# Performance work log

Measured on AMD Instinct MI355X. Metric: run time of the kernel, lower is better.

## Reference

```python
import jax, jax.numpy as jnp
import numpy as np

HEAD_SIZE = 128
EMBED_DIM = 1024
BLOCK = 2048


def setup_inputs() -> dict:
    key = jax.random.key(0)
    kx, kk, kq, kv = jax.random.split(key, 4)
    x = jax.random.normal(kx, (8, BLOCK, EMBED_DIM), dtype=jnp.float32)
    # nn.Linear weights stored as [out, in]; apply as x @ W.T -> keep as [in, out]
    s = 1.0 / np.sqrt(EMBED_DIM)
    W_key = jax.random.uniform(kk, (EMBED_DIM, HEAD_SIZE), jnp.float32, -s, s)
    W_query = jax.random.uniform(kq, (EMBED_DIM, HEAD_SIZE), jnp.float32, -s, s)
    W_value = jax.random.uniform(kv, (EMBED_DIM, HEAD_SIZE), jnp.float32, -s, s)
    return {"x": x, "W_key": W_key, "W_query": W_query, "W_value": W_value}


def reference(x, W_key, W_query, W_value):
    # NOTE: faithful to the source bug: q = self.key(x), W_query is unused.
    B, T, C = x.shape
    k = x @ W_key          # [B, T, H]
    q = x @ W_key          # [B, T, H]  (source uses key() for q too)
    scores = jnp.einsum("bqh,bkh->bqk", q, k) * (HEAD_SIZE ** -0.5)
    causal = jnp.tril(jnp.ones((T, T), dtype=bool))
    scores = jnp.where(causal, scores, -jnp.inf)
    weights = jax.nn.softmax(scores, axis=-1)
    v = x @ W_value        # [B, T, H]
    out = jnp.einsum("bqk,bkh->bqh", weights, v)
    return out
```

## Files before the change

### kernel.cpp

```cpp
#include <hip/hip_runtime.h>
#include <hip/hip_bf16.h>

typedef __attribute__((ext_vector_type(8))) short bf16x8;
typedef __attribute__((ext_vector_type(4))) short bf16x4;
typedef __attribute__((ext_vector_type(4))) float f32x4;

#define HS 128
#define ED 1024
#define TT 2048
#define NBATCH 8
#define NROWS (NBATCH * TT)
#define CHUNKS 4
#define TPC 8

__device__ __forceinline__ short bf16rne(float f) {
    unsigned u = __builtin_bit_cast(unsigned, f);
    u = u + 0x7fffu + ((u >> 16) & 1u);
    return (short)(u >> 16);
}

__device__ __forceinline__ void gl_lds16(const void* g, void* l) {
    __builtin_amdgcn_global_load_lds(
        (const __attribute__((address_space(1))) unsigned int*)g,
        (__attribute__((address_space(3))) unsigned int*)l, 16, 0, 0);
}

template <int NCALLS, int RBL2>
__device__ __forceinline__ void stage_tile(const char* gbase, void* lds,
                                           int gpitch, int tid, int wv) {
#pragma unroll
    for (int c = 0; c < NCALLS; ++c) {
        const int o = c * 4096 + tid * 16;
        const int row = o >> RBL2;
        const int colU = (o & ((1 << RBL2) - 1)) ^ ((row & 7) << 4);
        const char* g = gbase + (size_t)row * gpitch + colU;
        char* l = (char*)lds + c * 4096 + wv * 1024;
        gl_lds16(g, l);
    }
}

__device__ __forceinline__ bf16x8 lds_rd7(const short* lds, int row, int colE) {
    const int o = (row << 7) + (((colE * 2) & 127) ^ ((row & 7) << 4));
    return *reinterpret_cast<const bf16x8*>((const char*)lds + o);
}
__device__ __forceinline__ bf16x8 lds_rd8(const short* lds, int row, int colE) {
    const int o = (row << 8) + (((colE * 2) & 255) ^ ((row & 7) << 4));
    return *reinterpret_cast<const bf16x8*>((const char*)lds + o);
}

__global__ void k_wtrans(const float* __restrict__ Wk, const float* __restrict__ Wv,
                         short* __restrict__ WkT, short* __restrict__ WvT) {
    const float* W = blockIdx.y ? Wv : Wk;
    short* WT = blockIdx.y ? WvT : WkT;
    __shared__ float tile[16][128];
    const int k0 = blockIdx.x * 16;
    const int t = threadIdx.x;
#pragma unroll
    for (int i = 0; i < 8; ++i) {
        int idx = t + i * 256;
        tile[idx >> 7][idx & 127] = W[(size_t)(k0 + (idx >> 7)) * HS + (idx & 127)];
    }
    __syncthreads();
    const int n = t >> 1;
    const int h = (t & 1) * 8;
    bf16x8 o;
#pragma unroll
    for (int i = 0; i < 8; ++i) o[i] = bf16rne(tile[h + i][n]);
    *reinterpret_cast<bf16x8*>(&WT[(size_t)n * ED + k0 + h]) = o;
}

__global__ __launch_bounds__(256) void k_proj(
        const float* __restrict__ x,
        const short* __restrict__ WkT, const short* __restrict__ WvT,
        short* __restrict__ Kbuf, short* __restrict__ VT) {
    __shared__ short xl[2][64 * 64];
    __shared__ short wl[2][128 * 64];

    const int tid = threadIdx.x;
    const int lane = tid & 63;
    const int wv = tid >> 6;
    const int lr = lane & 15, g = lane >> 4;
    const int side = blockIdx.x;
    const int r0 = blockIdx.y * 64;
    const short* WT = side ? WvT : WkT;

    f32x4 acc[8];
#pragma unroll
    for (int i = 0; i < 8; ++i) acc[i] = (f32x4){0.f, 0.f, 0.f, 0.f};

    f32x4 xa[2][2];
    int xo[2], xrow[2], xcolU[2];
#pragma unroll
    for (int j = 0; j < 2; ++j) {
        xo[j] = tid * 32 + j * 16;
        xrow[j] = xo[j] >> 7;
        xcolU[j] = (xo[j] & 127) ^ ((xrow[j] & 7) << 4);
    }

#define XLOAD(s)                                                                    \
    {                                                                               \
        const int k0_ = (s) * 64;                                                   \
        _Pragma("unroll") for (int j = 0; j < 2; ++j) {                             \
            const float* sp = x + (size_t)(r0 + xrow[j]) * ED + k0_ + (xcolU[j] >> 1); \
            xa[j][0] = *reinterpret_cast<const f32x4*>(sp);                         \
            xa[j][1] = *reinterpret_cast<const f32x4*>(sp + 4);                     \
        }                                                                           \
    }
#define XWRITE(buf)                                                                 \
    {                                                                               \
        _Pragma("unroll") for (int j = 0; j < 2; ++j) {                             \
            bf16x8 pk;                                                              \
            _Pragma("unroll") for (int i = 0; i < 8; ++i)                           \
                pk[i] = bf16rne(xa[j][i >> 2][i & 3]);                              \
            *reinterpret_cast<bf16x8*>((char*)&xl[buf][0] + xo[j]) = pk;            \
        }                                                                           \
    }

    XLOAD(0);
    stage_tile<4, 7>((const char*)WT, &wl[0][0], ED * 2, tid, wv);
    XWRITE(0);
    __syncthreads();

    for (int s = 0; s < 16; ++s) {
        const int cur = s & 1;
        if (s + 1 < 16) {
            XLOAD(s + 1);
            stage_tile<4, 7>((const char*)WT + (size_t)(s + 1) * 128, &wl[cur ^ 1][0],
                             ED * 2, tid, wv);
        }
        bf16x8 af[2];
#pragma unroll
        for (int ks = 0; ks < 2; ++ks)
            af[ks] = lds_rd7(&xl[cur][0], wv * 16 + lr, ks * 32 + g * 8);
#pragma unroll
        for (int ks = 0; ks < 2; ++ks)
#pragma unroll
            for (int nf = 0; nf < 8; ++nf) {
                bf16x8 bfr = lds_rd7(&wl[cur][0], nf * 16 + lr, ks * 32 + g * 8);
                acc[nf] = __builtin_amdgcn_mfma_f32_16x16x32_bf16(af[ks], bfr, acc[nf], 0, 0, 0);
            }
        if (s + 1 < 16) XWRITE(cur ^ 1);
        __syncthreads();
    }
#undef XLOAD
#undef XWRITE

    const int mb = r0 + wv * 16 + 4 * g;
    if (side == 0) {
#pragma unroll
        for (int nf = 0; nf < 8; ++nf) {
            const int n = nf * 16 + lr;
#pragma unroll
            for (int r = 0; r < 4; ++r)
                Kbuf[(size_t)(mb + r) * HS + n] = bf16rne(acc[nf][r]);
        }
    } else {
        const int b = mb >> 11, tt = mb & (TT - 1);
#pragma unroll
        for (int nf = 0; nf < 8; ++nf) {
            const int n = nf * 16 + lr;
            bf16x4 o;
#pragma unroll
            for (int r = 0; r < 4; ++r) o[r] = bf16rne(acc[nf][r]);
            *reinterpret_cast<bf16x4*>(&VT[((size_t)b * HS + n) * TT + tt]) = o;
        }
    }
}

__global__ __launch_bounds__(256) void k_attn(
        const short* __restrict__ Kbuf, const short* __restrict__ VT,
        float* __restrict__ Opart, float* __restrict__ ml) {
    __shared__ short kl[2][64 * 128];
    __shared__ short vl[128 * 64];
    __shared__ short plds[4][16][72];

    const int tid = threadIdx.x;
    const int lane = tid & 63;
    const int wv = tid >> 6;
    const int lr = lane & 15, g = lane >> 4;

    const int bid = blockIdx.x;
    const int b = bid & 7;
    const int w = bid >> 3;
    int c, qt;
    if (w < 32)      { c = 0; qt = 31 - w; }
    else if (w < 56) { c = 1; qt = 31 - (w - 32); }
    else if (w < 72) { c = 2; qt = 31 - (w - 56); }
    else             { c = 3; qt = 31 - (w - 72); }
    const int t_begin = c * TPC;
    const int t_end = min(t_begin + TPC, qt + 1);

    const short* Kb = Kbuf + (size_t)b * TT * HS;
    const short* Vb = VT + (size_t)b * HS * TT;
    const int q0 = qt * 64 + wv * 16;

    bf16x8 qf[4];
#pragma unroll
    for (int ks = 0; ks < 4; ++ks)
        qf[ks] = *reinterpret_cast<const bf16x8*>(&Kb[(size_t)(q0 + lr) * HS + ks * 32 + g * 8]);

    stage_tile<4, 8>((const char*)(Kb + (size_t)t_begin * 64 * HS), &kl[0][0], HS * 2, tid, wv);
    __syncthreads();

    float mrun = -1e30f, lrun = 0.f;
    f32x4 oacc[8];
#pragma unroll
    for (int i = 0; i < 8; ++i) oacc[i] = (f32x4){0.f, 0.f, 0.f, 0.f};

    const float c1 = 0.08838834764831845f * 1.4426950408889634f;
    const int qrow = q0 + lr;
    int cur = 0;

    for (int t = t_begin; t < t_end; ++t) {
        const int kv0 = t * 64;
        stage_tile<4, 7>((const char*)(Vb + kv0), vl, TT * 2, tid, wv);
        if (t + 1 < t_end)
            stage_tile<4, 8>((const char*)(Kb + (size_t)(kv0 + 64) * HS), &kl[cur ^ 1][0],
                             HS * 2, tid, wv);

        f32x4 s[4];
#pragma unroll
        for (int i = 0; i < 4; ++i) s[i] = (f32x4){0.f, 0.f, 0.f, 0.f};
#pragma unroll
        for (int ks = 0; ks < 4; ++ks) {
            bf16x8 kf[4];
#pragma unroll
            for (int mf = 0; mf < 4; ++mf)
                kf[mf] = lds_rd8(&kl[cur][0], mf * 16 + lr, ks * 32 + g * 8);
#pragma unroll
            for (int mf = 0; mf < 4; ++mf)
                s[mf] = __builtin_amdgcn_mfma_f32_16x16x32_bf16(kf[mf], qf[ks], s[mf], 0, 0, 0);
        }
        float pv[4][4];
        float tmax = -1e30f;
#pragma unroll
        for (int mf = 0; mf < 4; ++mf)
#pragma unroll
            for (int r = 0; r < 4; ++r) {
                const int kv = kv0 + mf * 16 + 4 * g + r;
                float v = s[mf][r] * c1;
                v = (kv <= qrow) ? v : -1e30f;
                pv[mf][r] = v;
                tmax = fmaxf(tmax, v);
            }
        tmax = fmaxf(tmax, __shfl_xor(tmax, 16));
        tmax = fmaxf(tmax, __shfl_xor(tmax, 32));
        const float mnew = fmaxf(mrun, tmax);
        const float alpha = exp2f(mrun - mnew);
        mrun = mnew;
        float tsum = 0.f;
#pragma unroll
        for (int mf = 0; mf < 4; ++mf)
#pragma unroll
            for (int r = 0; r < 4; ++r) {
                const float p = exp2f(pv[mf][r] - mnew);
                pv[mf][r] = p;
                tsum += p;
            }
        tsum += __shfl_xor(tsum, 16);
        tsum += __shfl_xor(tsum, 32);
        lrun = lrun * alpha + tsum;
#pragma unroll
        for (int i = 0; i < 8; ++i) oacc[i] *= alpha;

        __syncthreads();

#pragma unroll
        for (int mf = 0; mf < 4; ++mf) {
            bf16x4 pk;
#pragma unroll
            for (int r = 0; r < 4; ++r) pk[r] = bf16rne(pv[mf][r]);
            *reinterpret_cast<bf16x4*>(&plds[wv][lr][mf * 16 + g * 4]) = pk;
        }
#pragma unroll
        for (int ks = 0; ks < 2; ++ks) {
            bf16x8 pf = *reinterpret_cast<const bf16x8*>(&plds[wv][lr][ks * 32 + g * 8]);
            bf16x8 vf[8];
#pragma unroll
            for (int mf = 0; mf < 8; ++mf)
                vf[mf] = lds_rd7(vl, mf * 16 + lr, ks * 32 + g * 8);
#pragma unroll
            for (int mf = 0; mf < 8; ++mf)
                oacc[mf] = __builtin_amdgcn_mfma_f32_16x16x32_bf16(vf[mf], pf, oacc[mf], 0, 0, 0);
        }
        __syncthreads();
        cur ^= 1;
    }

    const int row = b * TT + q0 + lr;
    const size_t pidx = (size_t)c * NROWS + row;
    float* op = Opart + pidx * HS;
#pragma unroll
    for (int mf = 0; mf < 8; ++mf)
        *reinterpret_cast<f32x4*>(&op[mf * 16 + g * 4]) = oacc[mf];
    if (lane < 16) {
        ml[pidx * 2] = mrun;
        ml[pidx * 2 + 1] = lrun;
    }
}

__global__ __launch_bounds__(256) void k_merge(const float* __restrict__ Opart,
                                               const float* __restrict__ ml,
                                               float* __restrict__ out) {
    const int idx = blockIdx.x * 256 + threadIdx.x;
    const int row = idx >> 5;
    const int h4 = (idx & 31) * 4;
    const int qt64 = (row & (TT - 1)) >> 6;
    const int nvalid = (qt64 >> 3) + 1;
    float m[CHUNKS], l[CHUNKS];
    float M = -1e30f;
#pragma unroll
    for (int c = 0; c < CHUNKS; ++c) {
        const bool valid = c < nvalid;
        const size_t p = (size_t)c * NROWS + row;
        m[c] = valid ? ml[p * 2] : -1e30f;
        l[c] = valid ? ml[p * 2 + 1] : 0.f;
        M = fmaxf(M, m[c]);
    }
    float denom = 0.f;
    f32x4 o = (f32x4){0.f, 0.f, 0.f, 0.f};
#pragma unroll
    for (int c = 0; c < CHUNKS; ++c) {
        const bool valid = c < nvalid;
        const float wgt = valid ? exp2f(m[c] - M) : 0.f;
        denom += wgt * l[c];
        if (valid) {
            f32x4 p = *reinterpret_cast<const f32x4*>(
                &Opart[((size_t)c * NROWS + row) * HS + h4]);
            o += p * wgt;
        }
    }
    const float inv = 1.0f / denom;
    *reinterpret_cast<f32x4*>(&out[(size_t)row * HS + h4]) = o * inv;
}

extern "C" void kernel_launch(void* const* d_in, const int* in_sizes, int n_in,
                              void* d_out, int out_size, void* d_ws, size_t ws_size,
                              hipStream_t stream) {
    (void)in_sizes; (void)n_in; (void)out_size; (void)ws_size;
    const float* x  = (const float*)d_in[0];
    const float* Wk = (const float*)d_in[1];
    const float* Wv = (const float*)d_in[3];
    float* out = (float*)d_out;

    char* ws = (char*)d_ws;
    short* Kbuf = (short*)ws;
    short* VT   = (short*)(ws + (size_t)NROWS * HS * 2);
    short* WkT  = (short*)(ws + 2 * (size_t)NROWS * HS * 2);
    short* WvT  = WkT + (size_t)HS * ED;
    float* Opart = (float*)(WvT + (size_t)HS * ED);
    float* mlb   = Opart + (size_t)CHUNKS * NROWS * HS;

    hipLaunchKernelGGL(k_wtrans, dim3(64, 2), dim3(256), 0, stream, Wk, Wv, WkT, WvT);
    hipLaunchKernelGGL(k_proj, dim3(2, NROWS / 64), dim3(256), 0, stream, x, WkT, WvT, Kbuf, VT);
    hipLaunchKernelGGL(k_attn, dim3(640), dim3(256), 0, stream, Kbuf, VT, Opart, mlb);
    hipLaunchKernelGGL(k_merge, dim3(NROWS * 32 / 256), dim3(256), 0, stream, Opart, mlb, out);
}
```

Measured before the change: 163.4 us.

## Double-buffer V tiles and deepen x prefetch in projection and attention kernels

In the projection kernel, x is now loaded two stages ahead into a second register set, and the bf16 conversion and LDS write happen before the MFMA work instead of after. The K-loop is fully unrolled, which adds register pressure. In the attention kernel, V gets its own double buffer prefetched together with the next K tile, and the mid-iteration barrier is removed. MFMA sections are also wrapped in s_setprio to favour matrix issue. This hides global load latency behind compute, at the cost of more LDS and registers, which could lower occupancy.

```diff
diff --git a/kernel.cpp b/kernel.cpp
--- a/kernel.cpp
+++ b/kernel.cpp
@@ -88,7 +88,6 @@
 #pragma unroll
     for (int i = 0; i < 8; ++i) acc[i] = (f32x4){0.f, 0.f, 0.f, 0.f};
 
-    f32x4 xa[2][2];
     int xo[2], xrow[2], xcolU[2];
 #pragma unroll
     for (int j = 0; j < 2; ++j) {
@@ -96,38 +95,41 @@
         xrow[j] = xo[j] >> 7;
         xcolU[j] = (xo[j] & 127) ^ ((xrow[j] & 7) << 4);
     }
-
-#define XLOAD(s)                                                                    \
-    {                                                                               \
-        const int k0_ = (s) * 64;                                                   \
-        _Pragma("unroll") for (int j = 0; j < 2; ++j) {                             \
-            const float* sp = x + (size_t)(r0 + xrow[j]) * ED + k0_ + (xcolU[j] >> 1); \
-            xa[j][0] = *reinterpret_cast<const f32x4*>(sp);                         \
-            xa[j][1] = *reinterpret_cast<const f32x4*>(sp + 4);                     \
-        }                                                                           \
-    }
-#define XWRITE(buf)                                                                 \
-    {                                                                               \
-        _Pragma("unroll") for (int j = 0; j < 2; ++j) {                             \
-            bf16x8 pk;                                                              \
-            _Pragma("unroll") for (int i = 0; i < 8; ++i)                           \
-                pk[i] = bf16rne(xa[j][i >> 2][i & 3]);                              \
-            *reinterpret_cast<bf16x8*>((char*)&xl[buf][0] + xo[j]) = pk;            \
-        }                                                                           \
-    }
-
-    XLOAD(0);
+    f32x4 xr[2][2][2];
+
+#define XLOAD(s, set)                                                                \
+    {                                                                                \
+        _Pragma("unroll") for (int j = 0; j < 2; ++j) {                              \
+            const float* sp = x + (size_t)(r0 + xrow[j]) * ED + (s) * 64 + (xcolU[j] >> 1); \
+            xr[set][j][0] = *reinterpret_cast<const f32x4*>(sp);                     \
+            xr[set][j][1] = *reinterpret_cast<const f32x4*>(sp + 4);                 \
+        }                                                                            \
+    }
+#define XWRITE(set, buf)                                                             \
+    {                                                                                \
+        _Pragma("unroll") for (int j = 0; j < 2; ++j) {                              \
+            bf16x8 pk;                                                               \
+            _Pragma("unroll") for (int i = 0; i < 8; ++i)                            \
+                pk[i] = bf16rne(xr[set][j][i >> 2][i & 3]);                          \
+            *reinterpret_cast<bf16x8*>((char*)&xl[buf][0] + xo[j]) = pk;             \
+        }                                                                            \
+    }
+
+    XLOAD(0, 0);
+    XLOAD(1, 1);
     stage_tile<4, 7>((const char*)WT, &wl[0][0], ED * 2, tid, wv);
-    XWRITE(0);
+    XWRITE(0, 0);
     __syncthreads();
 
+#pragma unroll
     for (int s = 0; s < 16; ++s) {
         const int cur = s & 1;
         if (s + 1 < 16) {
-            XLOAD(s + 1);
             stage_tile<4, 7>((const char*)WT + (size_t)(s + 1) * 128, &wl[cur ^ 1][0],
                              ED * 2, tid, wv);
-        }
+            XWRITE((s + 1) & 1, cur ^ 1);
+        }
+        if (s + 2 < 16) XLOAD(s + 2, cur);
         bf16x8 af[2];
 #pragma unroll
         for (int ks = 0; ks < 2; ++ks)
@@ -139,7 +141,6 @@
                 bf16x8 bfr = lds_rd7(&wl[cur][0], nf * 16 + lr, ks * 32 + g * 8);
                 acc[nf] = __builtin_amdgcn_mfma_f32_16x16x32_bf16(af[ks], bfr, acc[nf], 0, 0, 0);
             }
-        if (s + 1 < 16) XWRITE(cur ^ 1);
         __syncthreads();
     }
 #undef XLOAD
@@ -171,7 +172,7 @@
         const short* __restrict__ Kbuf, const short* __restrict__ VT,
         float* __restrict__ Opart, float* __restrict__ ml) {
     __shared__ short kl[2][64 * 128];
-    __shared__ short vl[128 * 64];
+    __shared__ short vl[2][128 * 64];
     __shared__ short plds[4][16][72];
 
     const int tid = threadIdx.x;
@@ -200,6 +201,7 @@
         qf[ks] = *reinterpret_cast<const bf16x8*>(&Kb[(size_t)(q0 + lr) * HS + ks * 32 + g * 8]);
 
     stage_tile<4, 8>((const char*)(Kb + (size_t)t_begin * 64 * HS), &kl[0][0], HS * 2, tid, wv);
+    stage_tile<4, 7>((const char*)(Vb + t_begin * 64), &vl[0][0], TT * 2, tid, wv);
     __syncthreads();
 
     float mrun = -1e30f, lrun = 0.f;
@@ -213,14 +215,16 @@
 
     for (int t = t_begin; t < t_end; ++t) {
         const int kv0 = t * 64;
-        stage_tile<4, 7>((const char*)(Vb + kv0), vl, TT * 2, tid, wv);
-        if (t + 1 < t_end)
+        if (t + 1 < t_end) {
             stage_tile<4, 8>((const char*)(Kb + (size_t)(kv0 + 64) * HS), &kl[cur ^ 1][0],
                              HS * 2, tid, wv);
+            stage_tile<4, 7>((const char*)(Vb + kv0 + 64), &vl[cur ^ 1][0], TT * 2, tid, wv);
+        }
 
         f32x4 s[4];
 #pragma unroll
         for (int i = 0; i < 4; ++i) s[i] = (f32x4){0.f, 0.f, 0.f, 0.f};
+        __builtin_amdgcn_s_setprio(1);
 #pragma unroll
         for (int ks = 0; ks < 4; ++ks) {
             bf16x8 kf[4];
@@ -231,6 +235,8 @@
             for (int mf = 0; mf < 4; ++mf)
                 s[mf] = __builtin_amdgcn_mfma_f32_16x16x32_bf16(kf[mf], qf[ks], s[mf], 0, 0, 0);
         }
+        __builtin_amdgcn_s_setprio(0);
+
         float pv[4][4];
         float tmax = -1e30f;
 #pragma unroll
@@ -263,8 +269,6 @@
 #pragma unroll
         for (int i = 0; i < 8; ++i) oacc[i] *= alpha;
 
-        __syncthreads();
-
 #pragma unroll
         for (int mf = 0; mf < 4; ++mf) {
             bf16x4 pk;
@@ -272,17 +276,20 @@
             for (int r = 0; r < 4; ++r) pk[r] = bf16rne(pv[mf][r]);
             *reinterpret_cast<bf16x4*>(&plds[wv][lr][mf * 16 + g * 4]) = pk;
         }
+        __builtin_amdgcn_s_setprio(1);
 #pragma unroll
         for (int ks = 0; ks < 2; ++ks) {
             bf16x8 pf = *reinterpret_cast<const bf16x8*>(&plds[wv][lr][ks * 32 + g * 8]);
             bf16x8 vf[8];
 #pragma unroll
             for (int mf = 0; mf < 8; ++mf)
-                vf[mf] = lds_rd7(vl, mf * 16 + lr, ks * 32 + g * 8);
+                vf[mf] = lds_rd7(&vl[cur][0], mf * 16 + lr, ks * 32 + g * 8);
 #pragma unroll
             for (int mf = 0; mf < 8; ++mf)
                 oacc[mf] = __builtin_amdgcn_mfma_f32_16x16x32_bf16(vf[mf], pf, oacc[mf], 0, 0, 0);
         }
+        __builtin_amdgcn_s_setprio(0);
+
         __syncthreads();
         cur ^= 1;
     }
```

New measurement: 165.3 us. No clear change (+1.1%).
